# Kernel tuning notes

Measured on AMD Instinct MI355X. Metric: run time of the kernel, lower is better.

Reference implementation:

```python
import math
import jax, jax.numpy as jnp
import numpy as np

B, LD, LE = 4, 1024, 1024
D, H, DK, DV, DFF, NL = 256, 8, 32, 32, 1024, 6


def _fixed_pos_emb(L, d):
    inv_freq = 1.0 / (10000.0 ** (jnp.arange(0, d, 2, dtype=jnp.float32) / d))
    pos = jnp.arange(L, dtype=jnp.float32)
    s = pos[:, None] * inv_freq[None, :]          # [L, d/2]
    return jnp.concatenate([jnp.sin(s), jnp.cos(s)], axis=-1)  # [L, d]


def _ln(x, g, b, eps=1e-5):
    m = x.mean(-1, keepdims=True)
    v = x.var(-1, keepdims=True)
    return (x - m) / jnp.sqrt(v + eps) * g + b


def _mha(x_q, x_kv, Wq, bq, Wk, bk, Wv, bv, Wo, bo, g, b, mask):
    Bq, Lq, _ = x_q.shape
    q = (x_q @ Wq + bq).reshape(Bq, Lq, H, DK).transpose(0, 2, 1, 3)   # [B,H,Lq,DK]
    k = (x_kv @ Wk + bk).reshape(Bq, -1, H, DK).transpose(0, 2, 1, 3)  # [B,H,Lk,DK]
    v = (x_kv @ Wv + bv).reshape(Bq, -1, H, DV).transpose(0, 2, 1, 3)  # [B,H,Lk,DV]
    scores = jnp.einsum('bhqd,bhkd->bhqk', q, k) / math.sqrt(DK)
    scores = jnp.where(mask[:, None, :, :], -1e9, scores)
    attn = jax.nn.softmax(scores, axis=-1)
    ctx = jnp.einsum('bhqk,bhkd->bhqd', attn, v)
    ctx = ctx.transpose(0, 2, 1, 3).reshape(Bq, Lq, H * DV)
    return _ln(ctx @ Wo + bo + x_q, g, b)


def _ffn(x, W1, b1, W2, b2, g, b):
    h = jax.nn.relu(x @ W1 + b1)   # conv1d k=1 == pointwise linear
    return _ln(h @ W2 + b2 + x, g, b)


def setup_inputs() -> dict:
    key = jax.random.key(0)
    ks = iter(jax.random.split(key, 40))
    def p(shape):
        return jax.random.normal(next(ks), shape, jnp.float32) * 0.02
    inp = {
        'enc_outputs': jax.random.normal(next(ks), (B, LE, D), jnp.float32),
        'dec_inputs': jax.random.normal(next(ks), (B, LD, 3), jnp.float32),
        'enc_masks': jnp.zeros((B, LE), jnp.int32),
        'dec_masks': jnp.zeros((B, LD), jnp.int32),
        'W_tgt': p((3, D)), 'b_tgt': jnp.zeros((D,), jnp.float32),
        'sa_Wq': p((NL, D, H * DK)), 'sa_bq': jnp.zeros((NL, H * DK), jnp.float32),
        'sa_Wk': p((NL, D, H * DK)), 'sa_bk': jnp.zeros((NL, H * DK), jnp.float32),
        'sa_Wv': p((NL, D, H * DV)), 'sa_bv': jnp.zeros((NL, H * DV), jnp.float32),
        'sa_Wo': p((NL, H * DV, D)), 'sa_bo': jnp.zeros((NL, D), jnp.float32),
        'sa_ln_g': jnp.ones((NL, D), jnp.float32), 'sa_ln_b': jnp.zeros((NL, D), jnp.float32),
        'ca_Wq': p((NL, D, H * DK)), 'ca_bq': jnp.zeros((NL, H * DK), jnp.float32),
        'ca_Wk': p((NL, D, H * DK)), 'ca_bk': jnp.zeros((NL, H * DK), jnp.float32),
        'ca_Wv': p((NL, D, H * DV)), 'ca_bv': jnp.zeros((NL, H * DV), jnp.float32),
        'ca_Wo': p((NL, H * DV, D)), 'ca_bo': jnp.zeros((NL, D), jnp.float32),
        'ca_ln_g': jnp.ones((NL, D), jnp.float32), 'ca_ln_b': jnp.zeros((NL, D), jnp.float32),
        'ff_W1': p((NL, D, DFF)), 'ff_b1': jnp.zeros((NL, DFF), jnp.float32),
        'ff_W2': p((NL, DFF, D)), 'ff_b2': jnp.zeros((NL, D), jnp.float32),
        'ff_ln_g': jnp.ones((NL, D), jnp.float32), 'ff_ln_b': jnp.zeros((NL, D), jnp.float32),
    }
    return inp


def reference(enc_outputs, dec_inputs, enc_masks, dec_masks, W_tgt, b_tgt,
              sa_Wq, sa_bq, sa_Wk, sa_bk, sa_Wv, sa_bv, sa_Wo, sa_bo, sa_ln_g, sa_ln_b,
              ca_Wq, ca_bq, ca_Wk, ca_bk, ca_Wv, ca_bv, ca_Wo, ca_bo, ca_ln_g, ca_ln_b,
              ff_W1, ff_b1, ff_W2, ff_b2, ff_ln_g, ff_ln_b):
    x = dec_inputs @ W_tgt + b_tgt                                  # tgt_emb
    pad = dec_masks[:, None, :].astype(bool)                        # [B,1,LD]
    causal = jnp.triu(jnp.ones((LD, LD), bool), 1)[None]            # [1,LD,LD]
    self_mask = pad | causal                                        # [B,LD,LD]
    cross_mask = jnp.broadcast_to(enc_masks[:, None, :].astype(bool), (x.shape[0], LD, LE))
    pe = _fixed_pos_emb(LD, D)[None]                                # [1,LD,D]
    for i in range(NL):
        x = x + pe                                                  # pos emb applied every layer (as in source)
        x = _mha(x, x, sa_Wq[i], sa_bq[i], sa_Wk[i], sa_bk[i], sa_Wv[i], sa_bv[i],
                 sa_Wo[i], sa_bo[i], sa_ln_g[i], sa_ln_b[i], self_mask)
        x = _mha(x, enc_outputs, ca_Wq[i], ca_bq[i], ca_Wk[i], ca_bk[i], ca_Wv[i], ca_bv[i],
                 ca_Wo[i], ca_bo[i], ca_ln_g[i], ca_ln_b[i], cross_mask)
        x = _ffn(x, ff_W1[i], ff_b1[i], ff_W2[i], ff_b2[i], ff_ln_g[i], ff_ln_b[i])
    return x
```

## Files before the change

kernel.cpp:

```cpp
#include <hip/hip_runtime.h>
#include <hip/hip_bf16.h>

#define B_   4
#define LD_  1024
#define LE_  1024
#define D_   256
#define H_   8
#define DK_  32
#define DFF_ 1024
#define NL_  6
#define NTOK (B_ * LD_)
#define M1E  1048576
#define WTOT 6291456

typedef __hip_bfloat16 bf16;
typedef __bf16 bf16_t;
typedef bf16_t bf16x8 __attribute__((ext_vector_type(8)));
typedef bf16_t bf16x4 __attribute__((ext_vector_type(4)));
typedef float  f32x4  __attribute__((ext_vector_type(4)));

__device__ __forceinline__ float bits2f(unsigned short u) {
    union { unsigned int i; float f; } w; w.i = ((unsigned int)u) << 16; return w.f;
}
__device__ __forceinline__ float ldx(const void* p, size_t i, int f32) {
    if (f32) return ((const float*)p)[i];
    return bits2f(((const unsigned short*)p)[i]);
}
__device__ __forceinline__ size_t afrag_idx(int m, int k, int K32) {
    return ((((size_t)(m >> 4) * K32 + (k >> 5)) * 64
             + (size_t)(((k >> 3) & 3) * 16 + (m & 15))) << 3) + (k & 7);
}

__global__ __launch_bounds__(256) void detect_kernel(
    const void* __restrict__ enc, int* __restrict__ flag)
{
    __shared__ int bad;
    if (threadIdx.x == 0) bad = 0;
    __syncthreads();
    const unsigned short* u = (const unsigned short*)enc;
    int b = 0;
    for (int i = threadIdx.x; i < 4096; i += 256) {
        unsigned short e = (u[i] >> 7) & 0xFF;
        if (e >= 142) b = 1;
    }
    if (b) atomicOr(&bad, 1);
    __syncthreads();
    if (threadIdx.x == 0) *flag = bad;
}

__global__ __launch_bounds__(256) void prep_w_kernel(
    const void* sWq, const void* sWk, const void* sWv, const void* sWo,
    const void* cWq, const void* cWk, const void* cWv, const void* cWo,
    const void* fW1, const void* fW2,
    bf16_t* __restrict__ Wf, const int* __restrict__ flag)
{
    const int f32 = *flag;
    const int g = blockIdx.x * 256 + threadIdx.x;
    const int li = g >> 17;
    int r = g & 131071;
    const void* src;
    size_t so;
    int N;
    if (r < 65536) {
        int t = r >> 13; r &= 8191;
        N = 256; so = (size_t)li * 65536;
        if      (t == 0) src = sWq; else if (t == 1) src = sWk;
        else if (t == 2) src = sWv; else if (t == 3) src = sWo;
        else if (t == 4) src = cWq; else if (t == 5) src = cWk;
        else if (t == 6) src = cWv; else             src = cWo;
    } else if (r < 98304) {
        r -= 65536; N = 1024; so = (size_t)li * 262144; src = fW1;
    } else {
        r -= 98304; N = 256;  so = (size_t)li * 262144; src = fW2;
    }
    const int lane = r & 63;
    const int q2 = r >> 6;
    int nb, kb;
    if (N == 256) { nb = q2 & 15; kb = q2 >> 4; }
    else          { nb = q2 & 63; kb = q2 >> 6; }
    const int k = kb * 32 + 8 * (lane >> 4);
    const int n = nb * 16 + (lane & 15);
    const size_t out = (size_t)g * 8;
#pragma unroll
    for (int j = 0; j < 8; ++j) {
        float v = ldx(src, so + (size_t)(k + j) * N + n, f32);
        bf16_t hv = (bf16_t)v;
        Wf[out + j] = hv;
        if (f32) Wf[WTOT + out + j] = (bf16_t)(v - (float)hv);
    }
}

__global__ __launch_bounds__(256) void pe_build_kernel(float* __restrict__ pe)
{
    int i = blockIdx.x * 256 + threadIdx.x;
    int d = i & (D_ - 1);
    int pos = i >> 8;
    int j = d & 127;
    float inv = powf(10000.0f, -2.0f * (float)j / (float)D_);
    float s = (float)pos * inv;
    pe[i] = (d < 128) ? sinf(s) : cosf(s);
}

__global__ __launch_bounds__(256) void embed_kernel(
    const void* __restrict__ dec, const void* __restrict__ Wt,
    const void* __restrict__ bt, float* __restrict__ x,
    bf16_t* __restrict__ xhi, bf16_t* __restrict__ xlo,
    const float* __restrict__ pe, const int* __restrict__ flag)
{
    int f32 = *flag;
    int i = blockIdx.x * 256 + threadIdx.x;
    int d = i & (D_ - 1);
    int t = i >> 8;
    float a0 = ldx(dec, t * 3 + 0, f32);
    float a1 = ldx(dec, t * 3 + 1, f32);
    float a2 = ldx(dec, t * 3 + 2, f32);
    float v = ldx(bt, d, f32) + a0 * ldx(Wt, 0 * D_ + d, f32)
            + a1 * ldx(Wt, 1 * D_ + d, f32) + a2 * ldx(Wt, 2 * D_ + d, f32)
            + pe[i & (LD_ * D_ - 1)];
    x[i] = v;
    size_t fi = afrag_idx(t, d, 8);
    bf16_t hv = (bf16_t)v;
    xhi[fi] = hv;
    xlo[fi] = (bf16_t)(v - (float)hv);
}

__global__ __launch_bounds__(256) void enc_split_kernel(
    const void* __restrict__ in, bf16_t* __restrict__ ehi, bf16_t* __restrict__ elo,
    const int* __restrict__ flag)
{
    int f32 = *flag;
    int i = blockIdx.x * 256 + threadIdx.x;
    int d = i & (D_ - 1);
    int t = i >> 8;
    float v = ldx(in, i, f32);
    size_t fi = afrag_idx(t, d, 8);
    bf16_t hv = (bf16_t)v;
    ehi[fi] = hv;
    elo[fi] = (bf16_t)(v - (float)hv);
}

__global__ __launch_bounds__(256) void gemmf_kernel(
    const bf16_t* __restrict__ Ah0, const bf16_t* __restrict__ Al0,
    const bf16_t* __restrict__ Ah1, const bf16_t* __restrict__ Al1,
    const bf16_t* __restrict__ Ah2, const bf16_t* __restrict__ Al2,
    const bf16_t* __restrict__ Wf, size_t wfBase, size_t wzStr,
    const void* __restrict__ b0, const void* __restrict__ b1,
    const void* __restrict__ b2, size_t bOff,
    bf16_t* __restrict__ C0, bf16_t* __restrict__ C1,
    bf16_t* __restrict__ C2, bf16_t* __restrict__ Cl,
    int M, int N, int K, int mode, const int* __restrict__ flag)
{
    const int f32 = *flag;
    const int z = blockIdx.z;
    const bf16_t* Ah = (z == 0) ? Ah0 : (z == 1) ? Ah1 : Ah2;
    const bf16_t* Al = (z == 0) ? Al0 : (z == 1) ? Al1 : Al2;
    const void* bias = (z == 0) ? b0 : (z == 1) ? b1 : b2;
    bf16_t* Cb = (z == 0) ? C0 : (z == 1) ? C1 : C2;

    const int tid = threadIdx.x;
    const int m0 = blockIdx.y * 32, n0 = blockIdx.x * 64;
    const int w = tid >> 6, l = tid & 63, l15 = l & 15, lg = l >> 4;
    const int wr = w >> 1, wc = w & 1;

    const bf16_t* wfp = Wf + wfBase + (size_t)z * wzStr;
    const int nbT = N >> 4;
    const int nb0 = (n0 >> 4) + 2 * wc;
    const int K32 = K >> 5;

    const int mb = (m0 >> 4) + wr;
    const bf16_t* ap  = Ah + ((size_t)mb * K32 * 64 + l) * 8;
    const bf16_t* alp = Al + ((size_t)mb * K32 * 64 + l) * 8;

    f32x4 acc0 = {0.f, 0.f, 0.f, 0.f};
    f32x4 acc1 = {0.f, 0.f, 0.f, 0.f};

    if (!f32) {
        f32x4 d0 = {0.f, 0.f, 0.f, 0.f};
        f32x4 d1 = {0.f, 0.f, 0.f, 0.f};
        bf16x8 A0, L0, P0, Q0, A1, L1, P1, Q1;
        bf16x8 A2, L2, P2, Q2, A3, L3, P3, Q3;
#define GF_LD(Ax, Lx, Px, Qx, KB) do {                                          \
        Ax = *(const bf16x8*)(ap + (size_t)(KB) * 512);                         \
        Lx = *(const bf16x8*)(alp + (size_t)(KB) * 512);                        \
        Px = *(const bf16x8*)(wfp + ((size_t)((KB) * nbT + nb0) * 64 + l) * 8); \
        Qx = *(const bf16x8*)(wfp + ((size_t)((KB) * nbT + nb0 + 1) * 64 + l) * 8); \
    } while (0)
#define GF_STEP(Ax, Lx, Px, Qx, KB) do {                                        \
        acc0 = __builtin_amdgcn_mfma_f32_16x16x32_bf16(Ax, Px, acc0, 0, 0, 0);  \
        acc1 = __builtin_amdgcn_mfma_f32_16x16x32_bf16(Ax, Qx, acc1, 0, 0, 0);  \
        d0   = __builtin_amdgcn_mfma_f32_16x16x32_bf16(Lx, Px, d0,   0, 0, 0);  \
        d1   = __builtin_amdgcn_mfma_f32_16x16x32_bf16(Lx, Qx, d1,   0, 0, 0);  \
        if ((KB) + 4 < K32) GF_LD(Ax, Lx, Px, Qx, (KB) + 4);                    \
    } while (0)
        GF_LD(A0, L0, P0, Q0, 0);
        GF_LD(A1, L1, P1, Q1, 1);
        GF_LD(A2, L2, P2, Q2, 2);
        GF_LD(A3, L3, P3, Q3, 3);
        for (int kb = 0; kb < K32; kb += 4) {
            GF_STEP(A0, L0, P0, Q0, kb);
            GF_STEP(A1, L1, P1, Q1, kb + 1);
            GF_STEP(A2, L2, P2, Q2, kb + 2);
            GF_STEP(A3, L3, P3, Q3, kb + 3);
        }
#undef GF_LD
#undef GF_STEP
#pragma unroll
        for (int r = 0; r < 4; ++r) { acc0[r] += d0[r]; acc1[r] += d1[r]; }
    } else {
        const bf16_t* wlp = wfp + WTOT;
        for (int kb = 0; kb < K32; ++kb) {
            bf16x8 ah  = *(const bf16x8*)(ap + (size_t)kb * 512);
            bf16x8 al8 = *(const bf16x8*)(alp + (size_t)kb * 512);
            bf16x8 bh0 = *(const bf16x8*)(wfp + ((size_t)(kb * nbT + nb0) * 64 + l) * 8);
            bf16x8 bh1 = *(const bf16x8*)(wfp + ((size_t)(kb * nbT + nb0 + 1) * 64 + l) * 8);
            bf16x8 bl0 = *(const bf16x8*)(wlp + ((size_t)(kb * nbT + nb0) * 64 + l) * 8);
            bf16x8 bl1 = *(const bf16x8*)(wlp + ((size_t)(kb * nbT + nb0 + 1) * 64 + l) * 8);
            acc0 = __builtin_amdgcn_mfma_f32_16x16x32_bf16(ah, bh0, acc0, 0, 0, 0);
            acc0 = __builtin_amdgcn_mfma_f32_16x16x32_bf16(al8, bh0, acc0, 0, 0, 0);
            acc0 = __builtin_amdgcn_mfma_f32_16x16x32_bf16(ah, bl0, acc0, 0, 0, 0);
            acc1 = __builtin_amdgcn_mfma_f32_16x16x32_bf16(ah, bh1, acc1, 0, 0, 0);
            acc1 = __builtin_amdgcn_mfma_f32_16x16x32_bf16(al8, bh1, acc1, 0, 0, 0);
            acc1 = __builtin_amdgcn_mfma_f32_16x16x32_bf16(ah, bl1, acc1, 0, 0, 0);
        }
    }

    const int cm = m0 + 16 * wr + 4 * lg;
    const int cn = n0 + 32 * wc + l15;
    const float b0v = ldx(bias, bOff + cn, f32);
    const float b1v = ldx(bias, bOff + cn + 16, f32);
    if (mode == 2) {
#pragma unroll
        for (int r = 0; r < 4; ++r) {
#pragma unroll
            for (int cc = 0; cc < 2; ++cc) {
                float v = (cc == 0 ? acc0[r] : acc1[r]) + (cc == 0 ? b0v : b1v);
                v = fmaxf(v, 0.0f);
                size_t fi = afrag_idx(cm + r, cn + 16 * cc, 32);
                bf16_t hv = (bf16_t)v;
                C0[fi] = hv;
                Cl[fi] = (bf16_t)(v - (float)hv);
            }
        }
    } else {
        const float qs = (z == 0) ? 0.17677669529663687f : 1.0f;
#pragma unroll
        for (int r = 0; r < 4; ++r) {
            const int token = cm + r;
#pragma unroll
            for (int cc = 0; cc < 2; ++cc) {
                const int d = cn + 16 * cc;
                const float v = ((cc == 0 ? acc0[r] : acc1[r]) + (cc == 0 ? b0v : b1v)) * qs;
                if (z < 2) {
                    int bb = token >> 10, qw = (token >> 4) & 63, lt = token & 15;
                    int hh = d >> 5, lg2 = (d >> 3) & 3, jj = d & 7;
                    size_t base = ((size_t)((bb * 8 + hh) * 64 + qw)) * 1024
                                + (size_t)(lg2 * 16 + lt) * 8 + jj;
                    bf16_t hv = (bf16_t)v;
                    Cb[base]       = hv;
                    Cb[base + 512] = (bf16_t)(v - (float)hv);
                } else {
                    int bb = token >> 10, ktt = (token >> 6) & 15, c2 = (token >> 5) & 1;
                    int w32 = token & 31;
                    int lg2 = (w32 >> 2) & 3, jj = (w32 >> 4) * 4 + (w32 & 3);
                    int hh = d >> 5, dvh = (d >> 4) & 1, lt = d & 15;
                    size_t base = ((size_t)((bb * 8 + hh) * 16 + ktt)) * 2048
                                + c2 * 1024 + dvh * 512 + (size_t)(lg2 * 16 + lt) * 8 + jj;
                    Cb[base] = (bf16_t)v;
                }
            }
        }
    }
}

__global__ __launch_bounds__(1024) void gemmln_kernel(
    const bf16_t* __restrict__ Ah, const bf16_t* __restrict__ Al,
    const bf16_t* __restrict__ Wf, size_t wfBase,
    const void* __restrict__ bias, float* __restrict__ x,
    bf16_t* __restrict__ xhi, bf16_t* __restrict__ xlo,
    const void* __restrict__ g, const void* __restrict__ bt,
    size_t bOff, int K,
    const float* __restrict__ pe, int addpe, const int* __restrict__ flag)
{
    const int f32 = *flag;
    __shared__ float red1[16][16];
    __shared__ float red2[16][16];
    __shared__ float mrow[16], irow[16];

    const int tid = threadIdx.x;
    const int m0 = blockIdx.x * 16;
    const int w = tid >> 6, l = tid & 63, l15 = l & 15, lg = l >> 4;
    const int K32 = K >> 5;

    const bf16_t* ap  = Ah + ((size_t)blockIdx.x * K32 * 64 + l) * 8;
    const bf16_t* alp = Al + ((size_t)blockIdx.x * K32 * 64 + l) * 8;
    const bf16_t* wfp = Wf + wfBase;

    f32x4 acc = {0.f, 0.f, 0.f, 0.f};

    if (!f32) {
        f32x4 accB = {0.f, 0.f, 0.f, 0.f};
        bf16x8 A0, L0, B0, A1, L1, B1, A2, L2, B2, A3, L3, B3;
#define GL_LD(Ax, Lx, Bx, KB) do {                                              \
        Ax = *(const bf16x8*)(ap + (size_t)(KB) * 512);                         \
        Lx = *(const bf16x8*)(alp + (size_t)(KB) * 512);                        \
        Bx = *(const bf16x8*)(wfp + ((size_t)((KB) * 16 + w) * 64 + l) * 8);    \
    } while (0)
#define GL_STEP(Ax, Lx, Bx, KB) do {                                            \
        acc  = __builtin_amdgcn_mfma_f32_16x16x32_bf16(Ax, Bx, acc,  0, 0, 0);  \
        accB = __builtin_amdgcn_mfma_f32_16x16x32_bf16(Lx, Bx, accB, 0, 0, 0);  \
        if ((KB) + 4 < K32) GL_LD(Ax, Lx, Bx, (KB) + 4);                        \
    } while (0)
        GL_LD(A0, L0, B0, 0);
        GL_LD(A1, L1, B1, 1);
        GL_LD(A2, L2, B2, 2);
        GL_LD(A3, L3, B3, 3);
        for (int kb = 0; kb < K32; kb += 4) {
            GL_STEP(A0, L0, B0, kb);
            GL_STEP(A1, L1, B1, kb + 1);
            GL_STEP(A2, L2, B2, kb + 2);
            GL_STEP(A3, L3, B3, kb + 3);
        }
#undef GL_LD
#undef GL_STEP
#pragma unroll
        for (int r = 0; r < 4; ++r) acc[r] += accB[r];
    } else {
        const bf16_t* wlp = wfp + WTOT;
        for (int kb = 0; kb < K32; ++kb) {
            bf16x8 ah  = *(const bf16x8*)(ap + (size_t)kb * 512);
            bf16x8 al8 = *(const bf16x8*)(alp + (size_t)kb * 512);
            bf16x8 bh  = *(const bf16x8*)(wfp + ((size_t)(kb * 16 + w) * 64 + l) * 8);
            bf16x8 bl  = *(const bf16x8*)(wlp + ((size_t)(kb * 16 + w) * 64 + l) * 8);
            acc = __builtin_amdgcn_mfma_f32_16x16x32_bf16(ah, bh, acc, 0, 0, 0);
            acc = __builtin_amdgcn_mfma_f32_16x16x32_bf16(al8, bh, acc, 0, 0, 0);
            acc = __builtin_amdgcn_mfma_f32_16x16x32_bf16(ah, bl, acc, 0, 0, 0);
        }
    }

    const int c = 16 * w + l15;
    const float bv = ldx(bias, bOff + c, f32);
    f32x4 v;
    float s1[4], s2[4];
#pragma unroll
    for (int r = 0; r < 4; ++r) {
        int tok = m0 + 4 * lg + r;
        v[r] = acc[r] + bv + x[(size_t)tok * 256 + c];
        s1[r] = v[r];
        s2[r] = v[r] * v[r];
    }
#pragma unroll
    for (int r = 0; r < 4; ++r) {
        s1[r] += __shfl_xor(s1[r], 1);  s2[r] += __shfl_xor(s2[r], 1);
        s1[r] += __shfl_xor(s1[r], 2);  s2[r] += __shfl_xor(s2[r], 2);
        s1[r] += __shfl_xor(s1[r], 4);  s2[r] += __shfl_xor(s2[r], 4);
        s1[r] += __shfl_xor(s1[r], 8);  s2[r] += __shfl_xor(s2[r], 8);
    }
    if (l15 == 0) {
#pragma unroll
        for (int r = 0; r < 4; ++r) {
            red1[w][4 * lg + r] = s1[r];
            red2[w][4 * lg + r] = s2[r];
        }
    }
    __syncthreads();
    if (tid < 16) {
        float t1 = 0.f, t2 = 0.f;
#pragma unroll
        for (int ww = 0; ww < 16; ++ww) { t1 += red1[ww][tid]; t2 += red2[ww][tid]; }
        float mean = t1 * (1.0f / 256.0f);
        float var  = t2 * (1.0f / 256.0f) - mean * mean;
        mrow[tid] = mean;
        irow[tid] = 1.0f / sqrtf(var + 1e-5f);
    }
    __syncthreads();

    const float gv  = ldx(g,  bOff + c, f32);
    const float btv = ldx(bt, bOff + c, f32);
#pragma unroll
    for (int r = 0; r < 4; ++r) {
        int row = 4 * lg + r;
        int tok = m0 + row;
        float out = (v[r] - mrow[row]) * irow[row] * gv + btv;
        if (addpe) out += pe[(size_t)(tok & (LD_ - 1)) * 256 + c];
        x[(size_t)tok * 256 + c] = out;
        size_t fi = afrag_idx(tok, c, 8);
        bf16_t hv = (bf16_t)out;
        xhi[fi] = hv;
        xlo[fi] = (bf16_t)(out - (float)hv);
    }
}

__global__ __launch_bounds__(256) void fattn4_kernel(
    const bf16_t* __restrict__ Qf, const bf16_t* __restrict__ Kf,
    const bf16_t* __restrict__ Vf,
    bf16_t* __restrict__ Chi, bf16_t* __restrict__ Clo,
    const int* __restrict__ mask, int causal)
{
    const int tid = threadIdx.x;
    const int qt = (int)blockIdx.x ^ ((((int)blockIdx.z >> 1) & 1) << 3);
    const int h = blockIdx.y, b = blockIdx.z;
    const int w = tid >> 6, l = tid & 63, l15 = l & 15, lg = l >> 4;
    const int bh = b * H_ + h;

    const size_t qbase = ((size_t)(bh * 64 + qt * 4 + w)) * 1024 + l * 8;
    const bf16x8 qh = *(const bf16x8*)(Qf + qbase);
    const bf16x8 ql = *(const bf16x8*)(Qf + qbase + 512);
    const int q_global = qt * 64 + w * 16 + l15;

    const bf16_t* kp = Kf + (size_t)bh * 64 * 1024 + l * 8;
    const bf16_t* vp = Vf + (size_t)bh * 16 * 2048 + l * 8;
    const int*    mp = mask + b * 1024 + 4 * lg;

    float m = -3.0e38f, lsum = 0.0f;
    f32x4 o0 = {0.f, 0.f, 0.f, 0.f};
    f32x4 o1 = {0.f, 0.f, 0.f, 0.f};

    const int nkt = causal ? (qt + 1) : (LE_ / 64);

    bf16x8 kha[4], kla[4], vaa[4];  int4 mka[4];
    bf16x8 khb[4], klb[4], vab[4];  int4 mkb[4];

#define FA_LOAD(kh_, kl_, va_, mk_, KT) do {                                    \
    _Pragma("unroll")                                                           \
    for (int nt = 0; nt < 4; ++nt) {                                            \
        kh_[nt] = *(const bf16x8*)(kp + (size_t)(KT) * 4096 + nt * 1024);       \
        kl_[nt] = *(const bf16x8*)(kp + (size_t)(KT) * 4096 + nt * 1024 + 512); \
    }                                                                           \
    va_[0] = *(const bf16x8*)(vp + (size_t)(KT) * 2048);                        \
    va_[1] = *(const bf16x8*)(vp + (size_t)(KT) * 2048 + 1024);                 \
    va_[2] = *(const bf16x8*)(vp + (size_t)(KT) * 2048 + 512);                  \
    va_[3] = *(const bf16x8*)(vp + (size_t)(KT) * 2048 + 1536);                 \
    _Pragma("unroll")                                                           \
    for (int nt = 0; nt < 4; ++nt)                                              \
        mk_[nt] = *(const int4*)(mp + (KT) * 64 + nt * 16);                     \
} while (0)

#define FA_COMPUTE(kh_, kl_, va_, mk_, KT) do {                                 \
    f32x4 s[4];                                                                 \
    _Pragma("unroll")                                                           \
    for (int nt = 0; nt < 4; ++nt) {                                            \
        f32x4 acc = {0.f, 0.f, 0.f, 0.f};                                       \
        acc = __builtin_amdgcn_mfma_f32_16x16x32_bf16(kh_[nt], qh, acc, 0,0,0); \
        acc = __builtin_amdgcn_mfma_f32_16x16x32_bf16(kl_[nt], qh, acc, 0,0,0); \
        acc = __builtin_amdgcn_mfma_f32_16x16x32_bf16(kh_[nt], ql, acc, 0,0,0); \
        s[nt] = acc;                                                            \
    }                                                                           \
    float pm = -3.0e38f;                                                        \
    _Pragma("unroll")                                                           \
    for (int nt = 0; nt < 4; ++nt) {                                            \
        _Pragma("unroll")                                                       \
        for (int r = 0; r < 4; ++r) {                                           \
            int key = (KT) * 64 + 16 * nt + 4 * lg + r;                         \
            int mv = (r==0)?mk_[nt].x:(r==1)?mk_[nt].y:(r==2)?mk_[nt].z:mk_[nt].w; \
            bool dead = (mv != 0) || (causal && key > q_global);                \
            float v = dead ? -1e30f : s[nt][r];                                 \
            s[nt][r] = v;                                                       \
            pm = fmaxf(pm, v);                                                  \
        }                                                                       \
    }                                                                           \
    pm = fmaxf(pm, __shfl_xor(pm, 16));                                         \
    pm = fmaxf(pm, __shfl_xor(pm, 32));                                         \
    float mnew = fmaxf(m, pm);                                                  \
    float alpha = __expf(m - mnew);                                             \
    m = mnew;                                                                   \
    float psum = 0.f;                                                           \
    _Pragma("unroll")                                                           \
    for (int nt = 0; nt < 4; ++nt) {                                            \
        _Pragma("unroll")                                                       \
        for (int r = 0; r < 4; ++r) {                                           \
            float p = __expf(s[nt][r] - m);                                     \
            s[nt][r] = p;                                                       \
            psum += p;                                                          \
        }                                                                       \
    }                                                                           \
    psum += __shfl_xor(psum, 16);                                               \
    psum += __shfl_xor(psum, 32);                                               \
    lsum = lsum * alpha + psum;                                                 \
    _Pragma("unroll")                                                           \
    for (int r = 0; r < 4; ++r) { o0[r] *= alpha; o1[r] *= alpha; }             \
    bf16x8 pb0, pb1;                                                            \
    _Pragma("unroll")                                                           \
    for (int r = 0; r < 4; ++r) {                                               \
        pb0[r]     = (bf16_t)s[0][r];  pb0[4 + r] = (bf16_t)s[1][r];            \
        pb1[r]     = (bf16_t)s[2][r];  pb1[4 + r] = (bf16_t)s[3][r];            \
    }                                                                           \
    o0 = __builtin_amdgcn_mfma_f32_16x16x32_bf16(va_[0], pb0, o0, 0, 0, 0);     \
    o0 = __builtin_amdgcn_mfma_f32_16x16x32_bf16(va_[1], pb1, o0, 0, 0, 0);     \
    o1 = __builtin_amdgcn_mfma_f32_16x16x32_bf16(va_[2], pb0, o1, 0, 0, 0);     \
    o1 = __builtin_amdgcn_mfma_f32_16x16x32_bf16(va_[3], pb1, o1, 0, 0, 0);     \
} while (0)

    FA_LOAD(kha, kla, vaa, mka, 0);
    int kt = 0;
    for (; kt + 2 <= nkt; kt += 2) {
        FA_LOAD(khb, klb, vab, mkb, kt + 1);
        FA_COMPUTE(kha, kla, vaa, mka, kt);
        if (kt + 2 < nkt) FA_LOAD(kha, kla, vaa, mka, kt + 2);
        FA_COMPUTE(khb, klb, vab, mkb, kt + 1);
    }
    if (kt < nkt) FA_COMPUTE(kha, kla, vaa, mka, kt);

#undef FA_LOAD
#undef FA_COMPUTE

    const float inv = 1.0f / lsum;
    bf16x4 h0, l0, h1, l1;
#pragma unroll
    for (int r = 0; r < 4; ++r) {
        float f0 = o0[r] * inv;
        float f1 = o1[r] * inv;
        bf16_t hv0 = (bf16_t)f0;
        bf16_t hv1 = (bf16_t)f1;
        h0[r] = hv0;  l0[r] = (bf16_t)(f0 - (float)hv0);
        h1[r] = hv1;  l1[r] = (bf16_t)(f1 - (float)hv1);
    }
    const int mb = b * 64 + qt * 4 + w;
    const int lp0 = (lg >> 1) * 16 + l15;
    const int jb = 4 * (lg & 1);
    const size_t g0 = ((size_t)mb * 8 + h) * 64;
    const size_t i0 = (g0 + lp0) * 8 + jb;
    const size_t i1 = (g0 + lp0 + 32) * 8 + jb;
    *(bf16x4*)(Chi + i0) = h0;
    *(bf16x4*)(Chi + i1) = h1;
    *(bf16x4*)(Clo + i0) = l0;
    *(bf16x4*)(Clo + i1) = l1;
}

__global__ __launch_bounds__(256) void cast_kernel(
    const float* __restrict__ x, void* __restrict__ out, const int* __restrict__ flag)
{
    int f32 = *flag;
    int i = blockIdx.x * 256 + threadIdx.x;
    if (f32) ((float*)out)[i] = x[i];
    else ((bf16*)out)[i] = __float2bfloat16(x[i]);
}

extern "C" void kernel_launch(void* const* d_in, const int* in_sizes, int n_in,
                              void* d_out, int out_size, void* d_ws, size_t ws_size,
                              hipStream_t stream)
{
    const void* enc       = d_in[0];
    const void* dec       = d_in[1];
    const int*  enc_masks = (const int*)d_in[2];
    const int*  dec_masks = (const int*)d_in[3];
    const void* W_tgt = d_in[4];
    const void* b_tgt = d_in[5];
    const void* sa_Wq = d_in[6];
    const void* sa_bq = d_in[7];
    const void* sa_Wk = d_in[8];
    const void* sa_bk = d_in[9];
    const void* sa_Wv = d_in[10];
    const void* sa_bv = d_in[11];
    const void* sa_Wo = d_in[12];
    const void* sa_bo = d_in[13];
    const void* sa_ln_g = d_in[14];
    const void* sa_ln_b = d_in[15];
    const void* ca_Wq = d_in[16];
    const void* ca_bq = d_in[17];
    const void* ca_Wk = d_in[18];
    const void* ca_bk = d_in[19];
    const void* ca_Wv = d_in[20];
    const void* ca_bv = d_in[21];
    const void* ca_Wo = d_in[22];
    const void* ca_bo = d_in[23];
    const void* ca_ln_g = d_in[24];
    const void* ca_ln_b = d_in[25];
    const void* ff_W1 = d_in[26];
    const void* ff_b1 = d_in[27];
    const void* ff_W2 = d_in[28];
    const void* ff_b2 = d_in[29];
    const void* ff_ln_g = d_in[30];
    const void* ff_ln_b = d_in[31];

    const size_t M1 = (size_t)NTOK * D_;
    float* ws = (float*)d_ws;
    float*  x      = ws;
    bf16_t* xhi    = (bf16_t*)(ws + 1 * M1);
    bf16_t* xlo    = xhi + M1E;
    bf16_t* ctxhi  = (bf16_t*)(ws + 2 * M1);
    bf16_t* ctxlo  = ctxhi + M1E;
    bf16_t* enchi  = (bf16_t*)(ws + 3 * M1);
    bf16_t* enclo  = enchi + M1E;
    bf16_t* hhi    = (bf16_t*)(ws + 4 * M1);
    bf16_t* hlo    = (bf16_t*)(ws + 6 * M1);
    bf16_t* qbuf   = (bf16_t*)(ws + 8 * M1);
    bf16_t* kbuf   = (bf16_t*)(ws + 9 * M1);
    bf16_t* vtbuf  = (bf16_t*)(ws + 10 * M1);
    float*  pe     = ws + 10 * M1 + M1 / 2;
    int*    flag   = (int*)(ws + 10 * M1 + 3 * M1 / 4);
    bf16_t* Wf     = (bf16_t*)(ws + 11 * M1);

    const int nElem = NTOK * D_;

    detect_kernel<<<1, 256, 0, stream>>>(enc, flag);
    prep_w_kernel<<<3072, 256, 0, stream>>>(
        sa_Wq, sa_Wk, sa_Wv, sa_Wo, ca_Wq, ca_Wk, ca_Wv, ca_Wo,
        ff_W1, ff_W2, Wf, flag);
    pe_build_kernel<<<(LD_ * D_) / 256, 256, 0, stream>>>(pe);
    embed_kernel<<<nElem / 256, 256, 0, stream>>>(dec, W_tgt, b_tgt, x, xhi, xlo, pe, flag);
    enc_split_kernel<<<nElem / 256, 256, 0, stream>>>(enc, enchi, enclo, flag);

    dim3 gProj(D_ / 64, NTOK / 32, 3);
    dim3 gFF1(DFF_ / 64, NTOK / 32, 1);
    dim3 gAttn(LD_ / 64, H_, B_);

    for (int i = 0; i < NL_; ++i) {
        const size_t LB   = (size_t)i * 1048576;
        const size_t bOff = (size_t)i * D_;

        gemmf_kernel<<<gProj, 256, 0, stream>>>(
            xhi, xlo, xhi, xlo, xhi, xlo,
            Wf, LB, 65536, sa_bq, sa_bk, sa_bv, bOff,
            qbuf, kbuf, vtbuf, nullptr, NTOK, D_, D_, 1, flag);
        fattn4_kernel<<<gAttn, 256, 0, stream>>>(qbuf, kbuf, vtbuf, ctxhi, ctxlo, dec_masks, 1);
        gemmln_kernel<<<NTOK / 16, 1024, 0, stream>>>(
            ctxhi, ctxlo, Wf, LB + 3 * 65536, sa_bo, x, xhi, xlo,
            sa_ln_g, sa_ln_b, bOff, D_, pe, 0, flag);

        gemmf_kernel<<<gProj, 256, 0, stream>>>(
            xhi, xlo, enchi, enclo, enchi, enclo,
            Wf, LB + 4 * 65536, 65536, ca_bq, ca_bk, ca_bv, bOff,
            qbuf, kbuf, vtbuf, nullptr, NTOK, D_, D_, 1, flag);
        fattn4_kernel<<<gAttn, 256, 0, stream>>>(qbuf, kbuf, vtbuf, ctxhi, ctxlo, enc_masks, 0);
        gemmln_kernel<<<NTOK / 16, 1024, 0, stream>>>(
            ctxhi, ctxlo, Wf, LB + 7 * 65536, ca_bo, x, xhi, xlo,
            ca_ln_g, ca_ln_b, bOff, D_, pe, 0, flag);

        gemmf_kernel<<<gFF1, 256, 0, stream>>>(
            xhi, xlo, xhi, xlo, xhi, xlo,
            Wf, LB + 524288, 0, ff_b1, ff_b1, ff_b1, (size_t)i * DFF_,
            hhi, hhi, hhi, hlo, NTOK, DFF_, D_, 2, flag);
        gemmln_kernel<<<NTOK / 16, 1024, 0, stream>>>(
            hhi, hlo, Wf, LB + 786432, ff_b2, x, xhi, xlo,
            ff_ln_g, ff_ln_b, bOff, DFF_, pe, (i < NL_ - 1) ? 1 : 0, flag);
    }

    cast_kernel<<<nElem / 256, 256, 0, stream>>>(x, d_out, flag);
}
```

Before: 1.041 ms.

## Fuse FFN into one LDS kernel and hoist cross-attention K/V projections

Replaces the two-kernel FFN (FF1 GEMM writing a hi/lo hidden buffer, then GEMM+LN) with one kernel that keeps each 16-token hidden tile in LDS and runs W2, the residual and LayerNorm in place. The final-layer output cast is folded into that kernel. The cross-attention K/V projections of the layer-invariant encoder output for all six layers are computed in a single launch before the loop, so each layer only projects Q. The new kernels also skip the low-part weight MFMAs when the inputs are bf16. In exchange, every FFN block streams the full W1 and W2 on its own, which adds L2 traffic. The workspace also grows to hold the K/V buffers for all layers.

```diff
diff --git a/kernel.cpp b/kernel.cpp
--- a/kernel.cpp
+++ b/kernel.cpp
@@ -147,8 +147,8 @@
     const void* __restrict__ b0, const void* __restrict__ b1,
     const void* __restrict__ b2, size_t bOff,
     bf16_t* __restrict__ C0, bf16_t* __restrict__ C1,
-    bf16_t* __restrict__ C2, bf16_t* __restrict__ Cl,
-    int M, int N, int K, int mode, const int* __restrict__ flag)
+    bf16_t* __restrict__ C2,
+    int M, int N, int K, const int* __restrict__ flag)
 {
     const int f32 = *flag;
     const int z = blockIdx.z;
@@ -228,45 +228,112 @@
     const int cn = n0 + 32 * wc + l15;
     const float b0v = ldx(bias, bOff + cn, f32);
     const float b1v = ldx(bias, bOff + cn + 16, f32);
-    if (mode == 2) {
-#pragma unroll
-        for (int r = 0; r < 4; ++r) {
-#pragma unroll
-            for (int cc = 0; cc < 2; ++cc) {
-                float v = (cc == 0 ? acc0[r] : acc1[r]) + (cc == 0 ? b0v : b1v);
-                v = fmaxf(v, 0.0f);
-                size_t fi = afrag_idx(cm + r, cn + 16 * cc, 32);
+    const float qs = (z == 0) ? 0.17677669529663687f : 1.0f;
+#pragma unroll
+    for (int r = 0; r < 4; ++r) {
+        const int token = cm + r;
+#pragma unroll
+        for (int cc = 0; cc < 2; ++cc) {
+            const int d = cn + 16 * cc;
+            const float v = ((cc == 0 ? acc0[r] : acc1[r]) + (cc == 0 ? b0v : b1v)) * qs;
+            if (z < 2) {
+                int bb = token >> 10, qw = (token >> 4) & 63, lt = token & 15;
+                int hh = d >> 5, lg2 = (d >> 3) & 3, jj = d & 7;
+                size_t base = ((size_t)((bb * 8 + hh) * 64 + qw)) * 1024
+                            + (size_t)(lg2 * 16 + lt) * 8 + jj;
                 bf16_t hv = (bf16_t)v;
-                C0[fi] = hv;
-                Cl[fi] = (bf16_t)(v - (float)hv);
+                Cb[base]       = hv;
+                Cb[base + 512] = (bf16_t)(v - (float)hv);
+            } else {
+                int bb = token >> 10, ktt = (token >> 6) & 15, c2 = (token >> 5) & 1;
+                int w32 = token & 31;
+                int lg2 = (w32 >> 2) & 3, jj = (w32 >> 4) * 4 + (w32 & 3);
+                int hh = d >> 5, dvh = (d >> 4) & 1, lt = d & 15;
+                size_t base = ((size_t)((bb * 8 + hh) * 16 + ktt)) * 2048
+                            + c2 * 1024 + dvh * 512 + (size_t)(lg2 * 16 + lt) * 8 + jj;
+                Cb[base] = (bf16_t)v;
             }
         }
-    } else {
-        const float qs = (z == 0) ? 0.17677669529663687f : 1.0f;
-#pragma unroll
-        for (int r = 0; r < 4; ++r) {
-            const int token = cm + r;
-#pragma unroll
-            for (int cc = 0; cc < 2; ++cc) {
-                const int d = cn + 16 * cc;
-                const float v = ((cc == 0 ? acc0[r] : acc1[r]) + (cc == 0 ? b0v : b1v)) * qs;
-                if (z < 2) {
-                    int bb = token >> 10, qw = (token >> 4) & 63, lt = token & 15;
-                    int hh = d >> 5, lg2 = (d >> 3) & 3, jj = d & 7;
-                    size_t base = ((size_t)((bb * 8 + hh) * 64 + qw)) * 1024
-                                + (size_t)(lg2 * 16 + lt) * 8 + jj;
-                    bf16_t hv = (bf16_t)v;
-                    Cb[base]       = hv;
-                    Cb[base + 512] = (bf16_t)(v - (float)hv);
-                } else {
-                    int bb = token >> 10, ktt = (token >> 6) & 15, c2 = (token >> 5) & 1;
-                    int w32 = token & 31;
-                    int lg2 = (w32 >> 2) & 3, jj = (w32 >> 4) * 4 + (w32 & 3);
-                    int hh = d >> 5, dvh = (d >> 4) & 1, lt = d & 15;
-                    size_t base = ((size_t)((bb * 8 + hh) * 16 + ktt)) * 2048
-                                + c2 * 1024 + dvh * 512 + (size_t)(lg2 * 16 + lt) * 8 + jj;
-                    Cb[base] = (bf16_t)v;
-                }
+    }
+}
+
+__global__ __launch_bounds__(256) void gemmkv_kernel(
+    const bf16_t* __restrict__ Ah, const bf16_t* __restrict__ Al,
+    const bf16_t* __restrict__ Wf,
+    const void* __restrict__ bk, const void* __restrict__ bv,
+    bf16_t* __restrict__ kvK, bf16_t* __restrict__ kvV,
+    const int* __restrict__ flag)
+{
+    const int f32 = *flag;
+    const int L = blockIdx.z >> 1, which = blockIdx.z & 1;
+    const void* bias = which ? bv : bk;
+    const size_t bOff = (size_t)L * 256;
+    bf16_t* Cb = which ? (kvV + (size_t)L * M1E) : (kvK + (size_t)L * 2 * M1E);
+
+    const int tid = threadIdx.x;
+    const int m0 = blockIdx.y * 32, n0 = blockIdx.x * 64;
+    const int w = tid >> 6, l = tid & 63, l15 = l & 15, lg = l >> 4;
+    const int wr = w >> 1, wc = w & 1;
+
+    const bf16_t* wfp = Wf + (size_t)L * 1048576 + (size_t)(5 + which) * 65536;
+    const int nb0 = (n0 >> 4) + 2 * wc;
+
+    const int mb = (m0 >> 4) + wr;
+    const bf16_t* ap  = Ah + ((size_t)mb * 8 * 64 + l) * 8;
+    const bf16_t* alp = Al + ((size_t)mb * 8 * 64 + l) * 8;
+
+    f32x4 acc0 = {0.f, 0.f, 0.f, 0.f};
+    f32x4 acc1 = {0.f, 0.f, 0.f, 0.f};
+    f32x4 d0 = {0.f, 0.f, 0.f, 0.f};
+    f32x4 d1 = {0.f, 0.f, 0.f, 0.f};
+
+    for (int kb = 0; kb < 8; ++kb) {
+        bf16x8 ah  = *(const bf16x8*)(ap + (size_t)kb * 512);
+        bf16x8 al8 = *(const bf16x8*)(alp + (size_t)kb * 512);
+        bf16x8 bh0 = *(const bf16x8*)(wfp + ((size_t)(kb * 16 + nb0) * 64 + l) * 8);
+        bf16x8 bh1 = *(const bf16x8*)(wfp + ((size_t)(kb * 16 + nb0 + 1) * 64 + l) * 8);
+        acc0 = __builtin_amdgcn_mfma_f32_16x16x32_bf16(ah, bh0, acc0, 0, 0, 0);
+        acc1 = __builtin_amdgcn_mfma_f32_16x16x32_bf16(ah, bh1, acc1, 0, 0, 0);
+        d0   = __builtin_amdgcn_mfma_f32_16x16x32_bf16(al8, bh0, d0, 0, 0, 0);
+        d1   = __builtin_amdgcn_mfma_f32_16x16x32_bf16(al8, bh1, d1, 0, 0, 0);
+        if (f32) {
+            const bf16_t* wlp = wfp + WTOT;
+            bf16x8 bl0 = *(const bf16x8*)(wlp + ((size_t)(kb * 16 + nb0) * 64 + l) * 8);
+            bf16x8 bl1 = *(const bf16x8*)(wlp + ((size_t)(kb * 16 + nb0 + 1) * 64 + l) * 8);
+            acc0 = __builtin_amdgcn_mfma_f32_16x16x32_bf16(ah, bl0, acc0, 0, 0, 0);
+            acc1 = __builtin_amdgcn_mfma_f32_16x16x32_bf16(ah, bl1, acc1, 0, 0, 0);
+        }
+    }
+#pragma unroll
+    for (int r = 0; r < 4; ++r) { acc0[r] += d0[r]; acc1[r] += d1[r]; }
+
+    const int cm = m0 + 16 * wr + 4 * lg;
+    const int cn = n0 + 32 * wc + l15;
+    const float b0v = ldx(bias, bOff + cn, f32);
+    const float b1v = ldx(bias, bOff + cn + 16, f32);
+#pragma unroll
+    for (int r = 0; r < 4; ++r) {
+        const int token = cm + r;
+#pragma unroll
+        for (int cc = 0; cc < 2; ++cc) {
+            const int d = cn + 16 * cc;
+            const float v = (cc == 0 ? acc0[r] : acc1[r]) + (cc == 0 ? b0v : b1v);
+            if (which == 0) {
+                int bb = token >> 10, qw = (token >> 4) & 63, lt = token & 15;
+                int hh = d >> 5, lg2 = (d >> 3) & 3, jj = d & 7;
+                size_t base = ((size_t)((bb * 8 + hh) * 64 + qw)) * 1024
+                            + (size_t)(lg2 * 16 + lt) * 8 + jj;
+                bf16_t hv = (bf16_t)v;
+                Cb[base]       = hv;
+                Cb[base + 512] = (bf16_t)(v - (float)hv);
+            } else {
+                int bb = token >> 10, ktt = (token >> 6) & 15, c2 = (token >> 5) & 1;
+                int w32 = token & 31;
+                int lg2 = (w32 >> 2) & 3, jj = (w32 >> 4) * 4 + (w32 & 3);
+                int hh = d >> 5, dvh = (d >> 4) & 1, lt = d & 15;
+                size_t base = ((size_t)((bb * 8 + hh) * 16 + ktt)) * 2048
+                            + c2 * 1024 + dvh * 512 + (size_t)(lg2 * 16 + lt) * 8 + jj;
+                Cb[base] = (bf16_t)v;
             }
         }
     }
@@ -387,6 +454,167 @@
         bf16_t hv = (bf16_t)out;
         xhi[fi] = hv;
         xlo[fi] = (bf16_t)(out - (float)hv);
+    }
+}
+
+__global__ __launch_bounds__(1024) void ffn_kernel(
+    const bf16_t* __restrict__ Ah, const bf16_t* __restrict__ Al,
+    const bf16_t* __restrict__ Wf, size_t w1Base, size_t w2Base,
+    const void* __restrict__ b1, const void* __restrict__ b2,
+    size_t b1Off, size_t b2Off, float* __restrict__ x,
+    bf16_t* __restrict__ xhi, bf16_t* __restrict__ xlo,
+    const void* __restrict__ g, const void* __restrict__ bt,
+    const float* __restrict__ pe, int addpe,
+    void* __restrict__ finalOut, int writeFinal,
+    const int* __restrict__ flag)
+{
+    const int f32 = *flag;
+    __shared__ __align__(16) bf16_t Hhi[32][512];
+    __shared__ __align__(16) bf16_t Hlo[32][512];
+    __shared__ float red1[16][16];
+    __shared__ float red2[16][16];
+    __shared__ float mrow[16], irow[16];
+
+    const int tid = threadIdx.x;
+    const int m0 = blockIdx.x * 16;
+    const int w = tid >> 6, l = tid & 63, l15 = l & 15, lg = l >> 4;
+
+    const bf16_t* ap  = Ah + ((size_t)blockIdx.x * 8 * 64 + l) * 8;
+    const bf16_t* alp = Al + ((size_t)blockIdx.x * 8 * 64 + l) * 8;
+    const bf16_t* wfp1 = Wf + w1Base;
+
+    f32x4 a1c[4] = {{0,0,0,0},{0,0,0,0},{0,0,0,0},{0,0,0,0}};
+    f32x4 a1d[4] = {{0,0,0,0},{0,0,0,0},{0,0,0,0},{0,0,0,0}};
+    if (!f32) {
+        for (int kb = 0; kb < 8; ++kb) {
+            bf16x8 A = *(const bf16x8*)(ap + (size_t)kb * 512);
+            bf16x8 L = *(const bf16x8*)(alp + (size_t)kb * 512);
+#pragma unroll
+            for (int c = 0; c < 4; ++c) {
+                bf16x8 Bc = *(const bf16x8*)(wfp1 + ((size_t)(kb * 64 + 4 * w + c) * 64 + l) * 8);
+                a1c[c] = __builtin_amdgcn_mfma_f32_16x16x32_bf16(A, Bc, a1c[c], 0, 0, 0);
+                a1d[c] = __builtin_amdgcn_mfma_f32_16x16x32_bf16(L, Bc, a1d[c], 0, 0, 0);
+            }
+        }
+#pragma unroll
+        for (int c = 0; c < 4; ++c)
+#pragma unroll
+            for (int r = 0; r < 4; ++r) a1c[c][r] += a1d[c][r];
+    } else {
+        const bf16_t* wlp1 = wfp1 + WTOT;
+        for (int kb = 0; kb < 8; ++kb) {
+            bf16x8 A = *(const bf16x8*)(ap + (size_t)kb * 512);
+            bf16x8 L = *(const bf16x8*)(alp + (size_t)kb * 512);
+#pragma unroll
+            for (int c = 0; c < 4; ++c) {
+                bf16x8 Bc = *(const bf16x8*)(wfp1 + ((size_t)(kb * 64 + 4 * w + c) * 64 + l) * 8);
+                bf16x8 Blc = *(const bf16x8*)(wlp1 + ((size_t)(kb * 64 + 4 * w + c) * 64 + l) * 8);
+                a1c[c] = __builtin_amdgcn_mfma_f32_16x16x32_bf16(A, Bc, a1c[c], 0, 0, 0);
+                a1c[c] = __builtin_amdgcn_mfma_f32_16x16x32_bf16(L, Bc, a1c[c], 0, 0, 0);
+                a1c[c] = __builtin_amdgcn_mfma_f32_16x16x32_bf16(A, Blc, a1c[c], 0, 0, 0);
+            }
+        }
+    }
+#pragma unroll
+    for (int c = 0; c < 4; ++c) {
+        const int col = 64 * w + 16 * c + l15;
+        const float bv = ldx(b1, b1Off + col, f32);
+        const int kb = col >> 5;
+        const int kgrp = (col >> 3) & 3;
+        const int jj = col & 7;
+#pragma unroll
+        for (int r = 0; r < 4; ++r) {
+            float v = fmaxf(a1c[c][r] + bv, 0.0f);
+            int lane2 = kgrp * 16 + 4 * lg + r;
+            bf16_t hv = (bf16_t)v;
+            Hhi[kb][lane2 * 8 + jj] = hv;
+            Hlo[kb][lane2 * 8 + jj] = (bf16_t)(v - (float)hv);
+        }
+    }
+    __syncthreads();
+
+    const bf16_t* wfp2 = Wf + w2Base;
+    f32x4 acc = {0.f, 0.f, 0.f, 0.f};
+    if (!f32) {
+        f32x4 accB = {0.f, 0.f, 0.f, 0.f};
+#pragma unroll 4
+        for (int kb = 0; kb < 32; ++kb) {
+            bf16x8 A2 = *(const bf16x8*)&Hhi[kb][l * 8];
+            bf16x8 L2 = *(const bf16x8*)&Hlo[kb][l * 8];
+            bf16x8 B2 = *(const bf16x8*)(wfp2 + ((size_t)(kb * 16 + w) * 64 + l) * 8);
+            acc  = __builtin_amdgcn_mfma_f32_16x16x32_bf16(A2, B2, acc,  0, 0, 0);
+            accB = __builtin_amdgcn_mfma_f32_16x16x32_bf16(L2, B2, accB, 0, 0, 0);
+        }
+#pragma unroll
+        for (int r = 0; r < 4; ++r) acc[r] += accB[r];
+    } else {
+        const bf16_t* wlp2 = wfp2 + WTOT;
+        for (int kb = 0; kb < 32; ++kb) {
+            bf16x8 A2 = *(const bf16x8*)&Hhi[kb][l * 8];
+            bf16x8 L2 = *(const bf16x8*)&Hlo[kb][l * 8];
+            bf16x8 B2 = *(const bf16x8*)(wfp2 + ((size_t)(kb * 16 + w) * 64 + l) * 8);
+            bf16x8 Bl2 = *(const bf16x8*)(wlp2 + ((size_t)(kb * 16 + w) * 64 + l) * 8);
+            acc = __builtin_amdgcn_mfma_f32_16x16x32_bf16(A2, B2, acc, 0, 0, 0);
+            acc = __builtin_amdgcn_mfma_f32_16x16x32_bf16(L2, B2, acc, 0, 0, 0);
+            acc = __builtin_amdgcn_mfma_f32_16x16x32_bf16(A2, Bl2, acc, 0, 0, 0);
+        }
+    }
+
+    const int c = 16 * w + l15;
+    const float bv2 = ldx(b2, b2Off + c, f32);
+    f32x4 v;
+    float s1[4], s2[4];
+#pragma unroll
+    for (int r = 0; r < 4; ++r) {
+        int tok = m0 + 4 * lg + r;
+        v[r] = acc[r] + bv2 + x[(size_t)tok * 256 + c];
+        s1[r] = v[r];
+        s2[r] = v[r] * v[r];
+    }
+#pragma unroll
+    for (int r = 0; r < 4; ++r) {
+        s1[r] += __shfl_xor(s1[r], 1);  s2[r] += __shfl_xor(s2[r], 1);
+        s1[r] += __shfl_xor(s1[r], 2);  s2[r] += __shfl_xor(s2[r], 2);
+        s1[r] += __shfl_xor(s1[r], 4);  s2[r] += __shfl_xor(s2[r], 4);
+        s1[r] += __shfl_xor(s1[r], 8);  s2[r] += __shfl_xor(s2[r], 8);
+    }
+    if (l15 == 0) {
+#pragma unroll
+        for (int r = 0; r < 4; ++r) {
+            red1[w][4 * lg + r] = s1[r];
+            red2[w][4 * lg + r] = s2[r];
+        }
+    }
+    __syncthreads();
+    if (tid < 16) {
+        float t1 = 0.f, t2 = 0.f;
+#pragma unroll
+        for (int ww = 0; ww < 16; ++ww) { t1 += red1[ww][tid]; t2 += red2[ww][tid]; }
+        float mean = t1 * (1.0f / 256.0f);
+        float var  = t2 * (1.0f / 256.0f) - mean * mean;
+        mrow[tid] = mean;
+        irow[tid] = 1.0f / sqrtf(var + 1e-5f);
+    }
+    __syncthreads();
+
+    const float gv  = ldx(g,  b2Off + c, f32);
+    const float btv = ldx(bt, b2Off + c, f32);
+#pragma unroll
+    for (int r = 0; r < 4; ++r) {
+        int row = 4 * lg + r;
+        int tok = m0 + row;
+        float out = (v[r] - mrow[row]) * irow[row] * gv + btv;
+        if (addpe) out += pe[(size_t)(tok & (LD_ - 1)) * 256 + c];
+        size_t idx = (size_t)tok * 256 + c;
+        x[idx] = out;
+        size_t fi = afrag_idx(tok, c, 8);
+        bf16_t hv = (bf16_t)out;
+        xhi[fi] = hv;
+        xlo[fi] = (bf16_t)(out - (float)hv);
+        if (writeFinal) {
+            if (f32) ((float*)finalOut)[idx] = out;
+            else ((bf16*)finalOut)[idx] = __float2bfloat16(out);
+        }
     }
 }
 
@@ -526,15 +754,6 @@
     *(bf16x4*)(Clo + i1) = l1;
 }
 
-__global__ __launch_bounds__(256) void cast_kernel(
-    const float* __restrict__ x, void* __restrict__ out, const int* __restrict__ flag)
-{
-    int f32 = *flag;
-    int i = blockIdx.x * 256 + threadIdx.x;
-    if (f32) ((float*)out)[i] = x[i];
-    else ((bf16*)out)[i] = __float2bfloat16(x[i]);
-}
-
 extern "C" void kernel_launch(void* const* d_in, const int* in_sizes, int n_in,
                               void* d_out, int out_size, void* d_ws, size_t ws_size,
                               hipStream_t stream)
@@ -581,14 +800,14 @@
     bf16_t* ctxlo  = ctxhi + M1E;
     bf16_t* enchi  = (bf16_t*)(ws + 3 * M1);
     bf16_t* enclo  = enchi + M1E;
-    bf16_t* hhi    = (bf16_t*)(ws + 4 * M1);
-    bf16_t* hlo    = (bf16_t*)(ws + 6 * M1);
-    bf16_t* qbuf   = (bf16_t*)(ws + 8 * M1);
-    bf16_t* kbuf   = (bf16_t*)(ws + 9 * M1);
-    bf16_t* vtbuf  = (bf16_t*)(ws + 10 * M1);
-    float*  pe     = ws + 10 * M1 + M1 / 2;
-    int*    flag   = (int*)(ws + 10 * M1 + 3 * M1 / 4);
-    bf16_t* Wf     = (bf16_t*)(ws + 11 * M1);
+    bf16_t* qbuf   = (bf16_t*)(ws + 4 * M1);
+    bf16_t* kbuf   = (bf16_t*)(ws + 5 * M1);
+    bf16_t* vtbuf  = (bf16_t*)(ws + 6 * M1);
+    float*  pe     = ws + 6 * M1 + M1 / 2;
+    int*    flag   = (int*)(ws + 6 * M1 + 3 * M1 / 4);
+    bf16_t* Wf     = (bf16_t*)(ws + 7 * M1);
+    bf16_t* kvK    = (bf16_t*)(ws + 14 * M1);
+    bf16_t* kvV    = (bf16_t*)(ws + 20 * M1);
 
     const int nElem = NTOK * D_;
 
@@ -599,41 +818,41 @@
     pe_build_kernel<<<(LD_ * D_) / 256, 256, 0, stream>>>(pe);
     embed_kernel<<<nElem / 256, 256, 0, stream>>>(dec, W_tgt, b_tgt, x, xhi, xlo, pe, flag);
     enc_split_kernel<<<nElem / 256, 256, 0, stream>>>(enc, enchi, enclo, flag);
-
-    dim3 gProj(D_ / 64, NTOK / 32, 3);
-    dim3 gFF1(DFF_ / 64, NTOK / 32, 1);
+    gemmkv_kernel<<<dim3(4, 128, 12), 256, 0, stream>>>(
+        enchi, enclo, Wf, ca_bk, ca_bv, kvK, kvV, flag);
+
+    dim3 gProj3(D_ / 64, NTOK / 32, 3);
+    dim3 gProj1(D_ / 64, NTOK / 32, 1);
     dim3 gAttn(LD_ / 64, H_, B_);
 
     for (int i = 0; i < NL_; ++i) {
         const size_t LB   = (size_t)i * 1048576;
         const size_t bOff = (size_t)i * D_;
 
-        gemmf_kernel<<<gProj, 256, 0, stream>>>(
+        gemmf_kernel<<<gProj3, 256, 0, stream>>>(
             xhi, xlo, xhi, xlo, xhi, xlo,
             Wf, LB, 65536, sa_bq, sa_bk, sa_bv, bOff,
-            qbuf, kbuf, vtbuf, nullptr, NTOK, D_, D_, 1, flag);
+            qbuf, kbuf, vtbuf, NTOK, D_, D_, flag);
         fattn4_kernel<<<gAttn, 256, 0, stream>>>(qbuf, kbuf, vtbuf, ctxhi, ctxlo, dec_masks, 1);
         gemmln_kernel<<<NTOK / 16, 1024, 0, stream>>>(
             ctxhi, ctxlo, Wf, LB + 3 * 65536, sa_bo, x, xhi, xlo,
             sa_ln_g, sa_ln_b, bOff, D_, pe, 0, flag);
 
-        gemmf_kernel<<<gProj, 256, 0, stream>>>(
-            xhi, xlo, enchi, enclo, enchi, enclo,
-            Wf, LB + 4 * 65536, 65536, ca_bq, ca_bk, ca_bv, bOff,
-            qbuf, kbuf, vtbuf, nullptr, NTOK, D_, D_, 1, flag);
-        fattn4_kernel<<<gAttn, 256, 0, stream>>>(qbuf, kbuf, vtbuf, ctxhi, ctxlo, enc_masks, 0);
+        gemmf_kernel<<<gProj1, 256, 0, stream>>>(
+            xhi, xlo, xhi, xlo, xhi, xlo,
+            Wf, LB + 4 * 65536, 65536, ca_bq, ca_bq, ca_bq, bOff,
+            qbuf, qbuf, qbuf, NTOK, D_, D_, flag);
+        fattn4_kernel<<<gAttn, 256, 0, stream>>>(
+            qbuf, kvK + (size_t)i * 2 * M1E, kvV + (size_t)i * M1E,
+            ctxhi, ctxlo, enc_masks, 0);
         gemmln_kernel<<<NTOK / 16, 1024, 0, stream>>>(
             ctxhi, ctxlo, Wf, LB + 7 * 65536, ca_bo, x, xhi, xlo,
             ca_ln_g, ca_ln_b, bOff, D_, pe, 0, flag);
 
-        gemmf_kernel<<<gFF1, 256, 0, stream>>>(
-            xhi, xlo, xhi, xlo, xhi, xlo,
-            Wf, LB + 524288, 0, ff_b1, ff_b1, ff_b1, (size_t)i * DFF_,
-            hhi, hhi, hhi, hlo, NTOK, DFF_, D_, 2, flag);
-        gemmln_kernel<<<NTOK / 16, 1024, 0, stream>>>(
-            hhi, hlo, Wf, LB + 786432, ff_b2, x, xhi, xlo,
-            ff_ln_g, ff_ln_b, bOff, DFF_, pe, (i < NL_ - 1) ? 1 : 0, flag);
-    }
-
-    cast_kernel<<<nElem / 256, 256, 0, stream>>>(x, d_out, flag);
-}
+        ffn_kernel<<<NTOK / 16, 1024, 0, stream>>>(
+            xhi, xlo, Wf, LB + 524288, LB + 786432,
+            ff_b1, ff_b2, (size_t)i * DFF_, bOff, x, xhi, xlo,
+            ff_ln_g, ff_ln_b, pe, (i < NL_ - 1) ? 1 : 0,
+            d_out, (i == NL_ - 1) ? 1 : 0, flag);
+    }
+}
```

Measured after the change: 958.4 us. 7.9% less time.
